# Kernel tuning notes

Hardware: AMD Instinct MI355X
Metric: run time of the kernel (lower is better)

The kernel has to match this reference:

```python
import jax, jax.numpy as jnp
import numpy as np

B, C, H, W = 4, 256, 64, 64
DIV = 4
D = C // DIV  # 64


def setup_inputs() -> dict:
    key = jax.random.key(0)
    ks = jax.random.split(key, 10)
    s = 0.05
    return {
        "x": jax.random.normal(ks[0], (B, C, H, W), dtype=jnp.float32),
        "wq": jax.random.normal(ks[1], (D, C), dtype=jnp.float32) * s,
        "bq": jax.random.normal(ks[2], (D,), dtype=jnp.float32) * s,
        "wk": jax.random.normal(ks[3], (D, C), dtype=jnp.float32) * s,
        "bk": jax.random.normal(ks[4], (D,), dtype=jnp.float32) * s,
        "wv": jax.random.normal(ks[5], (D, C), dtype=jnp.float32) * s,
        "bv": jax.random.normal(ks[6], (D,), dtype=jnp.float32) * s,
        "wsa": jax.random.normal(ks[7], (C, D), dtype=jnp.float32) * s,
        "bsa": jax.random.normal(ks[8], (C,), dtype=jnp.float32) * s,
        "gamma": jnp.zeros((1,), dtype=jnp.float32) + 0.5,
    }


def reference(x, wq, bq, wk, bk, wv, bv, wsa, bsa, gamma):
    b, c, h, w = x.shape
    hw = h * w
    xf = x.reshape(b, c, hw)  # [b, c, hw]
    # 1x1 convs == per-pixel linear maps
    q = jnp.einsum('dc,bcn->bdn', wq, xf) + bq[None, :, None]  # [b, d, hw]
    k = jnp.einsum('dc,bcn->bdn', wk, xf) + bk[None, :, None]
    v = jnp.einsum('dc,bcn->bdn', wv, xf) + bv[None, :, None]
    # attn[b, i, j] = softmax_j( q[:, :, i] . k[:, :, j] )
    scores = jnp.einsum('bdi,bdj->bij', q, k)  # [b, hw, hw]
    attn = jax.nn.softmax(scores, axis=-1)
    # sa = v @ attn^T : sa[b, d, i] = sum_j v[b, d, j] * attn[b, i, j]
    sa = jnp.einsum('bdj,bij->bdi', v, attn)  # [b, d, hw]
    out = jnp.einsum('cd,bdn->bcn', wsa, sa) + bsa[None, :, None]  # [b, c, hw]
    out = out.reshape(b, c, h, w)
    return gamma[0] * out + x
```

## Files before the change

### kernel.cpp

```cpp
#include <hip/hip_runtime.h>
#include <hip/hip_bf16.h>

typedef short short8 __attribute__((ext_vector_type(8)));
typedef float f32x4  __attribute__((ext_vector_type(4)));

static constexpr int NB  = 4;
static constexpr int NC  = 256;
static constexpr int NHW = 4096;
static constexpr int ND  = 64;
static constexpr int SPLIT = 8;
static constexpr int JITER = NHW / 64 / SPLIT;
static constexpr float SHIFT = 12.0f;

__device__ inline float bfbits2f(unsigned short u) {
    union { unsigned int i; float f; } x; x.i = ((unsigned int)u) << 16; return x.f;
}

__global__ __launch_bounds__(256) void wcvt_kernel(
    const float* __restrict__ wq, const float* __restrict__ wk,
    const float* __restrict__ wv, const float* __restrict__ wsa,
    __hip_bfloat16* __restrict__ wqkv_bf, __hip_bfloat16* __restrict__ wsa_bf)
{
    const int idx = blockIdx.x * 256 + threadIdx.x;
    if (idx < 192 * 256) {
        const int row = idx >> 8, col = idx & 255;
        const float* src = row < 64 ? wq : (row < 128 ? wk : wv);
        wqkv_bf[idx] = __float2bfloat16(src[(row & 63) * 256 + col]);
    } else {
        const int i = idx - 192 * 256;
        wsa_bf[i] = __float2bfloat16(wsa[i]);
    }
}

__global__ __launch_bounds__(512) void qkv_kernel(
    const float* __restrict__ x, const __hip_bfloat16* __restrict__ wqkv,
    const float* __restrict__ bq, const float* __restrict__ bk,
    const float* __restrict__ bv,
    __hip_bfloat16* __restrict__ qt, __hip_bfloat16* __restrict__ kt,
    __hip_bfloat16* __restrict__ vd)
{
    const int b  = blockIdx.x;
    const int n0 = blockIdx.y * 32;
    __shared__ __align__(16) __hip_bfloat16 xs[32][256];
    __shared__ __align__(16) __hip_bfloat16 vt_s[64][40];
    __shared__ __align__(16) __hip_bfloat16 qs [32][72];
    __shared__ __align__(16) __hip_bfloat16 ks2[32][72];

    const int t  = threadIdx.x;
    const int tn = t & 31;
    const int cq = t >> 5;

    const float* xb = x + (size_t)b * NC * NHW + n0;
    #pragma unroll
    for (int kblk = 0; kblk < 4; ++kblk) {
        const int c0 = cq * 4 + kblk * 64;
        __hip_bfloat16 pk[4];
        #pragma unroll
        for (int j = 0; j < 4; ++j)
            pk[j] = __float2bfloat16(xb[(size_t)(c0 + j) * NHW + tn]);
        const int kk = (c0 >> 3) ^ (tn & 7);
        *(uint2*)&xs[tn][kk * 8 + (c0 & 7)] = *(uint2*)pk;
    }
    __syncthreads();

    const int w    = t >> 6;
    const int wm   = w >> 2;
    const int wn   = w & 3;
    const int lane = t & 63;
    const int c    = lane & 15;
    const int q    = lane >> 4;

    f32x4 acc[3];
    #pragma unroll
    for (int nt = 0; nt < 3; ++nt) acc[nt] = (f32x4){0.f, 0.f, 0.f, 0.f};

    const int row = wm * 16 + c;
    #pragma unroll
    for (int kc = 0; kc < 8; ++kc) {
        const int kk = (kc * 4 + q) ^ (row & 7);
        const short8 a = *(const short8*)&xs[row][kk * 8];
        #pragma unroll
        for (int nt = 0; nt < 3; ++nt) {
            const short8 bfr = *(const short8*)(wqkv
                + (size_t)(wn * 48 + nt * 16 + c) * 256 + kc * 32 + q * 8);
            acc[nt] = __builtin_amdgcn_mfma_f32_16x16x32_bf16(a, bfr, acc[nt], 0, 0, 0);
        }
    }

    #pragma unroll
    for (int nt = 0; nt < 3; ++nt) {
        const int j0   = wn * 48 + nt * 16;
        const int sel  = j0 >> 6;
        const int colr = (j0 & 63) + c;
        const float bias = (sel == 0 ? bq : (sel == 1 ? bk : bv))[colr];
        if (sel < 2) {
            __hip_bfloat16 (*dst)[72] = (sel == 0 ? qs : ks2);
            #pragma unroll
            for (int r = 0; r < 4; ++r)
                dst[wm * 16 + q * 4 + r][colr] =
                    __float2bfloat16(acc[nt][r] + bias);
        } else {
            #pragma unroll
            for (int r = 0; r < 4; ++r)
                vt_s[colr][wm * 16 + q * 4 + r] =
                    __float2bfloat16(acc[nt][r] + bias);
        }
    }
    __syncthreads();
    for (int task = t; task < 768; task += 512) {
        const int which = task >> 8;
        const int i = task & 255;
        if (which == 0) {
            const int d = i >> 2, nc8 = (i & 3) * 8;
            *(short8*)(vd + ((size_t)(b * ND) + d) * NHW + n0 + nc8) =
                *(const short8*)&vt_s[d][nc8];
        } else {
            __hip_bfloat16* dst = (which == 1) ? qt : kt;
            const __hip_bfloat16 (*src)[72] = (which == 1) ? qs : ks2;
            const int n = i >> 3, d8 = (i & 7) * 8;
            *(short8*)(dst + ((size_t)(b * NHW) + n0 + n) * ND + d8) =
                *(const short8*)&src[n][d8];
        }
    }
}

__global__ __launch_bounds__(256, 4) void attn_kernel(
    const __hip_bfloat16* __restrict__ qt,
    const __hip_bfloat16* __restrict__ kt,
    const __hip_bfloat16* __restrict__ vd,
    __hip_bfloat16* __restrict__ O_part, float* __restrict__ l_part)
{
    const int b  = blockIdx.x;
    const int q0 = blockIdx.y * 128;
    const int s  = blockIdx.z;

    __shared__ __align__(16) __hip_bfloat16 ks [64][72];
    __shared__ __align__(16) __hip_bfloat16 vts[64][72];
    __shared__ __align__(16) __hip_bfloat16 ps [4][32][72];

    const int t    = threadIdx.x;
    const int w    = t >> 6;
    const int lane = t & 63;
    const int c    = lane & 15;
    const int q    = lane >> 4;

    short8 qf[2][2];
    #pragma unroll
    for (int mt = 0; mt < 2; ++mt)
        #pragma unroll
        for (int ch = 0; ch < 2; ++ch)
            qf[mt][ch] = *(const short8*)(qt
                + ((size_t)(b * NHW) + q0 + w * 32 + mt * 16 + c) * ND
                + ch * 32 + q * 8);

    f32x4 O[2][4];
    #pragma unroll
    for (int mt = 0; mt < 2; ++mt)
        #pragma unroll
        for (int dt = 0; dt < 4; ++dt)
            O[mt][dt] = (f32x4){0.f, 0.f, 0.f, 0.f};
    float lsum[2] = {0.f, 0.f};

    const int row_s = t >> 3;
    const int c8    = (t & 7) * 8;
    short8 kpre[2], vpre[2];
    {
        const int j0 = s * (NHW / SPLIT);
        kpre[0] = *(const short8*)(kt + ((size_t)(b * NHW) + j0 + row_s) * ND + c8);
        kpre[1] = *(const short8*)(kt + ((size_t)(b * NHW) + j0 + 32 + row_s) * ND + c8);
        vpre[0] = *(const short8*)(vd + ((size_t)(b * ND) + row_s) * NHW + j0 + c8);
        vpre[1] = *(const short8*)(vd + ((size_t)(b * ND) + 32 + row_s) * NHW + j0 + c8);
    }

    for (int it = 0; it < JITER; ++it) {
        __syncthreads();
        *(short8*)&ks [row_s     ][c8] = kpre[0];
        *(short8*)&ks [32 + row_s][c8] = kpre[1];
        *(short8*)&vts[row_s     ][c8] = vpre[0];
        *(short8*)&vts[32 + row_s][c8] = vpre[1];
        if (it + 1 < JITER) {
            const int j0 = s * (NHW / SPLIT) + (it + 1) * 64;
            kpre[0] = *(const short8*)(kt + ((size_t)(b * NHW) + j0 + row_s) * ND + c8);
            kpre[1] = *(const short8*)(kt + ((size_t)(b * NHW) + j0 + 32 + row_s) * ND + c8);
            vpre[0] = *(const short8*)(vd + ((size_t)(b * ND) + row_s) * NHW + j0 + c8);
            vpre[1] = *(const short8*)(vd + ((size_t)(b * ND) + 32 + row_s) * NHW + j0 + c8);
        }
        __syncthreads();

        #pragma unroll
        for (int jt = 0; jt < 4; ++jt) {
            const short8 kf0 = *(const short8*)&ks[jt * 16 + c][q * 8];
            const short8 kf1 = *(const short8*)&ks[jt * 16 + c][32 + q * 8];
            #pragma unroll
            for (int mt = 0; mt < 2; ++mt) {
                f32x4 acc = (f32x4){0.f, 0.f, 0.f, 0.f};
                acc = __builtin_amdgcn_mfma_f32_16x16x32_bf16(kf0, qf[mt][0], acc, 0, 0, 0);
                acc = __builtin_amdgcn_mfma_f32_16x16x32_bf16(kf1, qf[mt][1], acc, 0, 0, 0);
                __hip_bfloat16 pk[4];
                float ls = 0.f;
                #pragma unroll
                for (int r = 0; r < 4; ++r) {
                    const float p = __expf(acc[r] - SHIFT);
                    ls += p;
                    pk[r] = __float2bfloat16(p);
                }
                lsum[mt] += ls;
                *(uint2*)&ps[w][mt * 16 + c][jt * 16 + q * 4] = *(uint2*)pk;
            }
        }

        short8 af[2][2];
        #pragma unroll
        for (int mt = 0; mt < 2; ++mt) {
            af[mt][0] = *(const short8*)&ps[w][mt * 16 + c][q * 8];
            af[mt][1] = *(const short8*)&ps[w][mt * 16 + c][32 + q * 8];
        }
        #pragma unroll
        for (int dt = 0; dt < 4; ++dt) {
            const short8 vf0 = *(const short8*)&vts[dt * 16 + c][q * 8];
            const short8 vf1 = *(const short8*)&vts[dt * 16 + c][32 + q * 8];
            #pragma unroll
            for (int mt = 0; mt < 2; ++mt) {
                O[mt][dt] = __builtin_amdgcn_mfma_f32_16x16x32_bf16(af[mt][0], vf0, O[mt][dt], 0, 0, 0);
                O[mt][dt] = __builtin_amdgcn_mfma_f32_16x16x32_bf16(af[mt][1], vf1, O[mt][dt], 0, 0, 0);
            }
        }
    }

    const size_t sb = (size_t)(s * NB + b);
    #pragma unroll
    for (int mt = 0; mt < 2; ++mt) {
        float lv = lsum[mt];
        lv += __shfl_xor(lv, 16);
        lv += __shfl_xor(lv, 32);
        if (lane < 16)
            l_part[sb * NHW + q0 + w * 32 + mt * 16 + c] = lv;
    }
    #pragma unroll
    for (int mt = 0; mt < 2; ++mt)
        #pragma unroll
        for (int dt = 0; dt < 4; ++dt)
            #pragma unroll
            for (int r = 0; r < 4; ++r) {
                const int row = q0 + w * 32 + mt * 16 + q * 4 + r;
                O_part[(sb * NHW + row) * ND + dt * 16 + c] =
                    __float2bfloat16(O[mt][dt][r]);
            }
}

__global__ __launch_bounds__(512) void out_kernel(
    const __hip_bfloat16* __restrict__ O_part, const float* __restrict__ l_part,
    const __hip_bfloat16* __restrict__ wsa_bf,
    const float* __restrict__ bsa, const float* __restrict__ g,
    const float* __restrict__ x, float* __restrict__ out)
{
    const int b  = blockIdx.x;
    const int n0 = blockIdx.y * 32;
    const int t  = threadIdx.x;

    __shared__ __align__(16) __hip_bfloat16 sat_s[32][72];
    __shared__ __align__(16) float os[256][33];

    {
        const int n  = t >> 4;
        const int d4 = (t & 15) * 4;
        const size_t bn = (size_t)b * NHW + n0 + n;
        float num[4] = {0.f, 0.f, 0.f, 0.f};
        float den = 0.f;
        #pragma unroll
        for (int s = 0; s < SPLIT; ++s) {
            den += l_part[(size_t)s * NB * NHW + bn];
            const unsigned short* op = (const unsigned short*)(O_part
                + ((size_t)s * NB * NHW + bn) * ND + d4);
            ushort4 u = *(const ushort4*)op;
            num[0] += bfbits2f(u.x); num[1] += bfbits2f(u.y);
            num[2] += bfbits2f(u.z); num[3] += bfbits2f(u.w);
        }
        const float inv = 1.f / den;
        __hip_bfloat16 o4[4];
        #pragma unroll
        for (int j = 0; j < 4; ++j) o4[j] = __float2bfloat16(num[j] * inv);
        *(uint2*)&sat_s[n][d4] = *(uint2*)o4;
    }
    __syncthreads();

    {
        const int w    = t >> 6;
        const int lane = t & 63;
        const int c    = lane & 15;
        const int q    = lane >> 4;

        short8 bfr[2][2];
        #pragma unroll
        for (int nt = 0; nt < 2; ++nt)
            #pragma unroll
            for (int ch = 0; ch < 2; ++ch)
                bfr[nt][ch] = *(const short8*)&sat_s[nt * 16 + c][ch * 32 + q * 8];

        short8 af[2][2];
        #pragma unroll
        for (int mt = 0; mt < 2; ++mt)
            #pragma unroll
            for (int ch = 0; ch < 2; ++ch)
                af[mt][ch] = *(const short8*)(wsa_bf
                    + ((size_t)(w * 32 + mt * 16 + c)) * ND + ch * 32 + q * 8);

        #pragma unroll
        for (int mt = 0; mt < 2; ++mt) {
            float biasr[4];
            #pragma unroll
            for (int r = 0; r < 4; ++r)
                biasr[r] = bsa[w * 32 + mt * 16 + q * 4 + r];
            #pragma unroll
            for (int nt = 0; nt < 2; ++nt) {
                f32x4 a = (f32x4){0.f, 0.f, 0.f, 0.f};
                a = __builtin_amdgcn_mfma_f32_16x16x32_bf16(af[mt][0], bfr[nt][0], a, 0, 0, 0);
                a = __builtin_amdgcn_mfma_f32_16x16x32_bf16(af[mt][1], bfr[nt][1], a, 0, 0, 0);
                #pragma unroll
                for (int r = 0; r < 4; ++r)
                    os[w * 32 + mt * 16 + q * 4 + r][nt * 16 + c] = a[r] + biasr[r];
            }
        }
    }
    __syncthreads();

    const float gamma = g[0];
    #pragma unroll
    for (int pass = 0; pass < 4; ++pass) {
        const int row = pass * 64 + (t >> 3);
        const int nq  = (t & 7) * 4;
        const size_t oi = ((size_t)(b * NC) + row) * NHW + n0 + nq;
        const float4 xv = *(const float4*)(x + oi);
        float4 ov;
        ov.x = gamma * os[row][nq + 0] + xv.x;
        ov.y = gamma * os[row][nq + 1] + xv.y;
        ov.z = gamma * os[row][nq + 2] + xv.z;
        ov.w = gamma * os[row][nq + 3] + xv.w;
        *(float4*)(out + oi) = ov;
    }
}

extern "C" void kernel_launch(void* const* d_in, const int* in_sizes, int n_in,
                              void* d_out, int out_size, void* d_ws, size_t ws_size,
                              hipStream_t stream)
{
    const float* x     = (const float*)d_in[0];
    const float* wq    = (const float*)d_in[1];
    const float* bq    = (const float*)d_in[2];
    const float* wk    = (const float*)d_in[3];
    const float* bk    = (const float*)d_in[4];
    const float* wv    = (const float*)d_in[5];
    const float* bv    = (const float*)d_in[6];
    const float* wsa   = (const float*)d_in[7];
    const float* bsa   = (const float*)d_in[8];
    const float* gamma = (const float*)d_in[9];
    float* out = (float*)d_out;

    char* p = (char*)d_ws;
    __hip_bfloat16* wqkv_bf = (__hip_bfloat16*)p; p += (size_t)128 << 10;
    __hip_bfloat16* wsa_bf  = (__hip_bfloat16*)p; p += (size_t)128 << 10;
    __hip_bfloat16* qt = (__hip_bfloat16*)p; p += (size_t)2 << 20;
    __hip_bfloat16* kt = (__hip_bfloat16*)p; p += (size_t)2 << 20;
    __hip_bfloat16* vd = (__hip_bfloat16*)p; p += (size_t)2 << 20;
    __hip_bfloat16* O_part = (__hip_bfloat16*)p; p += (size_t)16 << 20;
    float* l_part = (float*)p; p += (size_t)1 << 20;

    wcvt_kernel<<<dim3(256), 256, 0, stream>>>(wq, wk, wv, wsa, wqkv_bf, wsa_bf);
    qkv_kernel<<<dim3(NB, NHW / 32), 512, 0, stream>>>(
        x, wqkv_bf, bq, bk, bv, qt, kt, vd);
    attn_kernel<<<dim3(NB, NHW / 128, SPLIT), 256, 0, stream>>>(
        qt, kt, vd, O_part, l_part);
    out_kernel<<<dim3(NB, NHW / 32), 512, 0, stream>>>(
        O_part, l_part, wsa_bf, bsa, gamma, x, out);
}
```

Baseline: 133.9 us.

## Double-buffer K/V via direct global-to-LDS loads with XOR swizzle in attention

The attention kernel now loads K and V tiles straight into double-buffered LDS with global_load_lds, in place of staging them through registers. This removes one of the two barriers per iteration and the register round trip. Padding is replaced by an XOR swizzle on both the K/V buffers and the P scratch to avoid bank conflicts. The P tile is processed in two 32-column halves, which halves its LDS footprint. The risks are correctness of the async LDS loads without an explicit vmcnt wait before the barrier, and the larger shared memory use of the double buffers.

```diff
diff --git a/kernel.cpp b/kernel.cpp
--- a/kernel.cpp
+++ b/kernel.cpp
@@ -3,6 +3,7 @@
 
 typedef short short8 __attribute__((ext_vector_type(8)));
 typedef float f32x4  __attribute__((ext_vector_type(4)));
+typedef unsigned int u32;
 
 static constexpr int NB  = 4;
 static constexpr int NC  = 256;
@@ -14,6 +15,12 @@
 
 __device__ inline float bfbits2f(unsigned short u) {
     union { unsigned int i; float f; } x; x.i = ((unsigned int)u) << 16; return x.f;
+}
+
+__device__ static inline void gload16(const void* g, void* l) {
+    __builtin_amdgcn_global_load_lds(
+        (const __attribute__((address_space(1))) u32*)g,
+        (__attribute__((address_space(3))) u32*)l, 16, 0, 0);
 }
 
 __global__ __launch_bounds__(256) void wcvt_kernel(
@@ -134,15 +141,23 @@
     const int q0 = blockIdx.y * 128;
     const int s  = blockIdx.z;
 
-    __shared__ __align__(16) __hip_bfloat16 ks [64][72];
-    __shared__ __align__(16) __hip_bfloat16 vts[64][72];
-    __shared__ __align__(16) __hip_bfloat16 ps [4][32][72];
+    __shared__ __align__(16) __hip_bfloat16 kbuf[2][64][64];
+    __shared__ __align__(16) __hip_bfloat16 vbuf[2][64][64];
+    __shared__ __align__(16) __hip_bfloat16 ps[4][32][32];
 
     const int t    = threadIdx.x;
     const int w    = t >> 6;
     const int lane = t & 63;
     const int c    = lane & 15;
     const int q    = lane >> 4;
+    const int sw   = c & 7;
+
+    const int rl   = lane >> 3;
+    const int u    = lane & 7;
+    const int swz8 = ((u ^ rl) & 7) * 8;
+
+    const __hip_bfloat16* kt_b = kt + (size_t)b * NHW * ND;
+    const __hip_bfloat16* vd_b = vd + (size_t)b * ND * NHW;
 
     short8 qf[2][2];
     #pragma unroll
@@ -161,70 +176,75 @@
             O[mt][dt] = (f32x4){0.f, 0.f, 0.f, 0.f};
     float lsum[2] = {0.f, 0.f};
 
-    const int row_s = t >> 3;
-    const int c8    = (t & 7) * 8;
-    short8 kpre[2], vpre[2];
-    {
-        const int j0 = s * (NHW / SPLIT);
-        kpre[0] = *(const short8*)(kt + ((size_t)(b * NHW) + j0 + row_s) * ND + c8);
-        kpre[1] = *(const short8*)(kt + ((size_t)(b * NHW) + j0 + 32 + row_s) * ND + c8);
-        vpre[0] = *(const short8*)(vd + ((size_t)(b * ND) + row_s) * NHW + j0 + c8);
-        vpre[1] = *(const short8*)(vd + ((size_t)(b * ND) + 32 + row_s) * NHW + j0 + c8);
-    }
+    const int j0base = s * (NHW / SPLIT);
+
+    #pragma unroll
+    for (int i = 0; i < 2; ++i) {
+        const int r0 = w * 16 + i * 8;
+        gload16(kt_b + (size_t)(j0base + r0 + rl) * ND + swz8, &kbuf[0][r0][0]);
+        gload16(vd_b + (size_t)(r0 + rl) * NHW + j0base + swz8, &vbuf[0][r0][0]);
+    }
+    __syncthreads();
 
     for (int it = 0; it < JITER; ++it) {
+        const int cur = it & 1;
+        if (it + 1 < JITER) {
+            const int j0 = j0base + (it + 1) * 64;
+            #pragma unroll
+            for (int i = 0; i < 2; ++i) {
+                const int r0 = w * 16 + i * 8;
+                gload16(kt_b + (size_t)(j0 + r0 + rl) * ND + swz8,
+                        &kbuf[cur ^ 1][r0][0]);
+                gload16(vd_b + (size_t)(r0 + rl) * NHW + j0 + swz8,
+                        &vbuf[cur ^ 1][r0][0]);
+            }
+        }
+
+        #pragma unroll
+        for (int jh = 0; jh < 2; ++jh) {
+            #pragma unroll
+            for (int jtl = 0; jtl < 2; ++jtl) {
+                const int rk = (jh * 2 + jtl) * 16 + c;
+                const int u0 = q ^ sw;
+                const short8 kf0 = *(const short8*)&kbuf[cur][rk][u0 * 8];
+                const short8 kf1 = *(const short8*)&kbuf[cur][rk][(u0 ^ 4) * 8];
+                #pragma unroll
+                for (int mt = 0; mt < 2; ++mt) {
+                    f32x4 acc = (f32x4){0.f, 0.f, 0.f, 0.f};
+                    acc = __builtin_amdgcn_mfma_f32_16x16x32_bf16(kf0, qf[mt][0], acc, 0, 0, 0);
+                    acc = __builtin_amdgcn_mfma_f32_16x16x32_bf16(kf1, qf[mt][1], acc, 0, 0, 0);
+                    __hip_bfloat16 pk[4];
+                    float ls = 0.f;
+                    #pragma unroll
+                    for (int r = 0; r < 4; ++r) {
+                        const float p = __expf(acc[r] - SHIFT);
+                        ls += p;
+                        pk[r] = __float2bfloat16(p);
+                    }
+                    lsum[mt] += ls;
+                    *(uint2*)&ps[w][mt * 16 + c][((jtl * 4 + q) ^ sw) * 4] =
+                        *(uint2*)pk;
+                }
+            }
+            short8 af[2];
+            #pragma unroll
+            for (int mt = 0; mt < 2; ++mt) {
+                union { uint2 u2[2]; short8 s8; } cv;
+                cv.u2[0] = *(const uint2*)&ps[w][mt * 16 + c][((2 * q)     ^ sw) * 4];
+                cv.u2[1] = *(const uint2*)&ps[w][mt * 16 + c][((2 * q + 1) ^ sw) * 4];
+                af[mt] = cv.s8;
+            }
+            #pragma unroll
+            for (int dt = 0; dt < 4; ++dt) {
+                const int rv = dt * 16 + c;
+                const short8 vf = *(const short8*)
+                    &vbuf[cur][rv][((jh * 4 + q) ^ sw) * 8];
+                #pragma unroll
+                for (int mt = 0; mt < 2; ++mt)
+                    O[mt][dt] = __builtin_amdgcn_mfma_f32_16x16x32_bf16(af[mt], vf, O[mt][dt], 0, 0, 0);
+            }
+        }
         __syncthreads();
-        *(short8*)&ks [row_s     ][c8] = kpre[0];
-        *(short8*)&ks [32 + row_s][c8] = kpre[1];
-        *(short8*)&vts[row_s     ][c8] = vpre[0];
-        *(short8*)&vts[32 + row_s][c8] = vpre[1];
-        if (it + 1 < JITER) {
-            const int j0 = s * (NHW / SPLIT) + (it + 1) * 64;
-            kpre[0] = *(const short8*)(kt + ((size_t)(b * NHW) + j0 + row_s) * ND + c8);
-            kpre[1] = *(const short8*)(kt + ((size_t)(b * NHW) + j0 + 32 + row_s) * ND + c8);
-            vpre[0] = *(const short8*)(vd + ((size_t)(b * ND) + row_s) * NHW + j0 + c8);
-            vpre[1] = *(const short8*)(vd + ((size_t)(b * ND) + 32 + row_s) * NHW + j0 + c8);
-        }
-        __syncthreads();
-
-        #pragma unroll
-        for (int jt = 0; jt < 4; ++jt) {
-            const short8 kf0 = *(const short8*)&ks[jt * 16 + c][q * 8];
-            const short8 kf1 = *(const short8*)&ks[jt * 16 + c][32 + q * 8];
-            #pragma unroll
-            for (int mt = 0; mt < 2; ++mt) {
-                f32x4 acc = (f32x4){0.f, 0.f, 0.f, 0.f};
-                acc = __builtin_amdgcn_mfma_f32_16x16x32_bf16(kf0, qf[mt][0], acc, 0, 0, 0);
-                acc = __builtin_amdgcn_mfma_f32_16x16x32_bf16(kf1, qf[mt][1], acc, 0, 0, 0);
-                __hip_bfloat16 pk[4];
-                float ls = 0.f;
-                #pragma unroll
-                for (int r = 0; r < 4; ++r) {
-                    const float p = __expf(acc[r] - SHIFT);
-                    ls += p;
-                    pk[r] = __float2bfloat16(p);
-                }
-                lsum[mt] += ls;
-                *(uint2*)&ps[w][mt * 16 + c][jt * 16 + q * 4] = *(uint2*)pk;
-            }
-        }
-
-        short8 af[2][2];
-        #pragma unroll
-        for (int mt = 0; mt < 2; ++mt) {
-            af[mt][0] = *(const short8*)&ps[w][mt * 16 + c][q * 8];
-            af[mt][1] = *(const short8*)&ps[w][mt * 16 + c][32 + q * 8];
-        }
-        #pragma unroll
-        for (int dt = 0; dt < 4; ++dt) {
-            const short8 vf0 = *(const short8*)&vts[dt * 16 + c][q * 8];
-            const short8 vf1 = *(const short8*)&vts[dt * 16 + c][32 + q * 8];
-            #pragma unroll
-            for (int mt = 0; mt < 2; ++mt) {
-                O[mt][dt] = __builtin_amdgcn_mfma_f32_16x16x32_bf16(af[mt][0], vf0, O[mt][dt], 0, 0, 0);
-                O[mt][dt] = __builtin_amdgcn_mfma_f32_16x16x32_bf16(af[mt][1], vf1, O[mt][dt], 0, 0, 0);
-            }
-        }
     }
 
     const size_t sb = (size_t)(s * NB + b);
```

New measurement: 135.7 us. Within noise of the previous version (+1.4%).
